# Optimization experiments

Hardware: AMD Instinct MI355X
Metric: run time of the kernel (lower is better)

Reference implementation:

```python
import jax, jax.numpy as jnp
import numpy as np

B, N, F, T, K, C, CT = 64, 307, 64, 12, 3, 64, 64
LN_EPS = 1e-5


def setup_inputs() -> dict:
    key = jax.random.key(0)
    ks = jax.random.split(key, 20)
    s = 0.1  # mild scale so sigmoid/softmax stay in a sane range
    return {
        "x": jax.random.normal(ks[0], (B, N, F, T), jnp.float32),
        "W1": jax.random.normal(ks[1], (T,), jnp.float32) * s,
        "W2": jax.random.normal(ks[2], (F, T), jnp.float32) * s,
        "W3": jax.random.normal(ks[3], (F,), jnp.float32) * s,
        "b_s": jax.random.normal(ks[4], (1, N, N), jnp.float32) * s,
        "V_s": jax.random.normal(ks[5], (N, N), jnp.float32) * s,
        "U1": jax.random.normal(ks[6], (N,), jnp.float32) * s,
        "U2": jax.random.normal(ks[7], (F, N), jnp.float32) * s,
        "U3": jax.random.normal(ks[8], (F,), jnp.float32) * s,
        "b_e": jax.random.normal(ks[9], (1, T, T), jnp.float32) * s,
        "V_e": jax.random.normal(ks[10], (T, T), jnp.float32) * s,
        "cheb": jax.random.normal(ks[11], (K, N, N), jnp.float32) * s,
        "Theta": jax.random.normal(ks[12], (K, F, C), jnp.float32) * s,
        "tconv_w": jax.random.normal(ks[13], (CT, C, 1, 3), jnp.float32) * s,
        "tconv_b": jax.random.normal(ks[14], (CT,), jnp.float32) * s,
        "rconv_w": jax.random.normal(ks[15], (CT, F, 1, 1), jnp.float32) * s,
        "rconv_b": jax.random.normal(ks[16], (CT,), jnp.float32) * s,
        "gamma": jnp.ones((CT,), jnp.float32),
        "beta": jnp.zeros((CT,), jnp.float32),
    }


def _temporal_attention(x, U1, U2, U3, b_e, V_e):
    # x: (B,N,F,T)
    lhs = jnp.einsum('bnft,n->btf', x, U1) @ U2            # (B,T,N)
    rhs = jnp.einsum('f,bnft->bnt', U3, x)                 # (B,N,T)
    prod = jnp.einsum('btn,bns->bts', lhs, rhs)            # (B,T,T)
    E = jnp.einsum('uv,bvt->but', V_e, jax.nn.sigmoid(prod + b_e))
    return jax.nn.softmax(E, axis=1)                       # (B,T,T)


def _spatial_attention(x, W1, W2, W3, b_s, V_s):
    # x: (B,N,F,T)
    lhs = jnp.einsum('bnft,t->bnf', x, W1) @ W2            # (B,N,T)
    rhs = jnp.einsum('f,bnft->btn', W3, x)                 # (B,T,N)
    prod = jnp.einsum('bnt,btm->bnm', lhs, rhs)            # (B,N,N)
    sig = jax.nn.sigmoid(prod + b_s)                       # (B,N,N)
    # torch: (V_s @ sig.T(1,2,0)).T(2,0,1) -> S[b,a,i] = sum_v V_s[i,v]*sig[b,a,v]
    S = jnp.einsum('bav,iv->bai', sig, V_s)
    return jax.nn.softmax(S, axis=1)                       # (B,N,N)


def _cheb_conv_sat(x, S, cheb, Theta):
    # x: (B,N,F,T), S: (B,N,N), cheb: (K,N,N), Theta: (K,F,C)
    A = cheb[:, None] * S[None]                            # (K,B,N,N) attention-masked polys
    # out[b,j,c,t] = sum_{k,i,f} A[k,b,i,j] * x[b,i,f,t] * Theta[k,f,c]
    rhs = jnp.einsum('kbij,bift->kbjft', A, x)             # (K,B,N,F,T)
    out = jnp.einsum('kbjft,kfc->bjct', rhs, Theta)        # (B,N,C,T)
    return jax.nn.relu(out)


def _conv2d(inp, w, b, pad):
    # inp: (B,C_in,N,T), w: (C_out,C_in,kh,kw)
    y = jax.lax.conv_general_dilated(
        inp, w, window_strides=(1, 1), padding=pad,
        dimension_numbers=('NCHW', 'OIHW', 'NCHW'))
    return y + b[None, :, None, None]


def reference(x, W1, W2, W3, b_s, V_s, U1, U2, U3, b_e, V_e,
              cheb, Theta, tconv_w, tconv_b, rconv_w, rconv_b, gamma, beta):
    b, n, f_, t = x.shape
    # temporal attention gating
    E = _temporal_attention(x, U1, U2, U3, b_e, V_e)                      # (B,T,T)
    x_TAt = (x.reshape(b, n * f_, t) @ E).reshape(b, n, f_, t)
    # spatial attention on temporally-gated signal
    S = _spatial_attention(x_TAt, W1, W2, W3, b_s, V_s)                   # (B,N,N)
    # attention-weighted Chebyshev graph conv on original x
    spatial_gcn = _cheb_conv_sat(x, S, cheb, Theta)                       # (B,N,C,T)
    # temporal conv (1,3), SAME padding along time
    tco = _conv2d(spatial_gcn.transpose(0, 2, 1, 3), tconv_w, tconv_b,
                  ((0, 0), (1, 1))).transpose(0, 2, 1, 3)                 # (B,N,CT,T)
    # 1x1 residual conv on x
    res = _conv2d(x.transpose(0, 2, 1, 3), rconv_w, rconv_b,
                  ((0, 0), (0, 0))).transpose(0, 2, 1, 3)                 # (B,N,CT,T)
    h = jax.nn.relu(res + tco)
    # LayerNorm over the filter/channel axis (axis=2)
    mu = jnp.mean(h, axis=2, keepdims=True)
    var = jnp.var(h, axis=2, keepdims=True)
    hn = (h - mu) * jax.lax.rsqrt(var + LN_EPS)
    return hn * gamma[None, None, :, None] + beta[None, None, :, None]
```

## Files before the change

kernel.cpp:

```cpp
#include <hip/hip_runtime.h>
#include <hip/hip_bf16.h>
#include <math.h>

constexpr int B = 64, N = 307, F = 64, T = 12, K = 3, C = 64, CT = 64;
constexpr float LN_EPS = 1e-5f;
constexpr int FT = F * T;

typedef float vf4 __attribute__((ext_vector_type(4)));
typedef short s16x8 __attribute__((ext_vector_type(8)));

__device__ __forceinline__ unsigned short f2bf(float f) {
    unsigned int u = __float_as_uint(f);
    unsigned int r = u + 0x7FFFu + ((u >> 16) & 1u);
    return (unsigned short)(r >> 16);
}


__global__ void k_lhs1_e(const float* __restrict__ x, const float* __restrict__ U1,
                         float* __restrict__ out) {
    int bb = blockIdx.x;
    int b = bb / 3;
    int e = (bb % 3) * 256 + threadIdx.x;
    const float* xp = x + (size_t)b * N * FT + e;
    float s = 0.f;
    for (int n = 0; n < N; n++) s += xp[(size_t)n * FT] * U1[n];
    int f = e / T, t = e % T;
    out[((size_t)b * T + t) * F + f] = s;
}

__global__ void k_xdots(const float* __restrict__ x, const float* __restrict__ U3,
                        const float* __restrict__ W3, float* __restrict__ rhs_e,
                        float* __restrict__ xw3) {
    int idx = blockIdx.x * blockDim.x + threadIdx.x;
    if (idx >= B * N * T) return;
    int t = idx % T;
    size_t bn = idx / T;
    const float* xp = x + bn * F * T + t;
    float s1 = 0.f, s2 = 0.f;
    for (int f = 0; f < F; f++) {
        float v = xp[f * T];
        s1 += U3[f] * v;
        s2 += W3[f] * v;
    }
    rhs_e[idx] = s1;
    xw3[idx] = s2;
}

__global__ void k_lhs_e(const float* __restrict__ lhs1, const float* __restrict__ U2,
                        float* __restrict__ out) {
    int idx = blockIdx.x * blockDim.x + threadIdx.x;
    if (idx >= B * T * N) return;
    int n = idx % N;
    int bt = idx / N;
    const float* lp = lhs1 + (size_t)bt * F;
    float s = 0.f;
    for (int f = 0; f < F; f++) s += lp[f] * U2[f * N + n];
    out[idx] = s;
}

__global__ void k_tatt(const float* __restrict__ lhs, const float* __restrict__ rhs,
                       const float* __restrict__ b_e, const float* __restrict__ V_e,
                       const float* __restrict__ W1, float* __restrict__ E,
                       float* __restrict__ EW1) {
    int b = blockIdx.x;
    int tid = threadIdx.x;
    __shared__ float ll[T][N + 1];
    __shared__ float rr_[T][N + 1];
    __shared__ float sig[T * T];
    __shared__ float Ev[T * T];
    __shared__ float mx[T], sm[T];
    for (int l = tid; l < T * N; l += 256) ll[l / N][l % N] = lhs[(size_t)b * T * N + l];
    for (int l = tid; l < N * T; l += 256) rr_[l % T][l / T] = rhs[(size_t)b * N * T + l];
    __syncthreads();
    if (tid < T * T) {
        int t = tid % T, u = tid / T;
        const vf4* lp4 = (const vf4*)&ll[u][0];
        const vf4* rp4 = (const vf4*)&rr_[t][0];
        float s = 0.f;
#pragma unroll 4
        for (int q = 0; q < 76; q++) {
            vf4 a = lp4[q], c = rp4[q];
            s += a[0] * c[0] + a[1] * c[1] + a[2] * c[2] + a[3] * c[3];
        }
        for (int n = 304; n < N; n++) s += ll[u][n] * rr_[t][n];
        s += b_e[u * T + t];
        sig[tid] = 1.f / (1.f + expf(-s));
    }
    __syncthreads();
    if (tid < T * T) {
        int t = tid % T, u = tid / T;
        float e = 0.f;
        for (int v = 0; v < T; v++) e += V_e[u * T + v] * sig[v * T + t];
        Ev[tid] = e;
    }
    __syncthreads();
    if (tid < T) {
        float m = -1e30f;
        for (int u = 0; u < T; u++) m = fmaxf(m, Ev[u * T + tid]);
        float s = 0.f;
        for (int u = 0; u < T; u++) s += expf(Ev[u * T + tid] - m);
        mx[tid] = m;
        sm[tid] = s;
    }
    __syncthreads();
    if (tid < T * T) {
        int t = tid % T;
        float val = expf(Ev[tid] - mx[t]) / sm[t];
        E[(size_t)b * T * T + tid] = val;
        sig[tid] = val;
    }
    __syncthreads();
    if (tid < T) {
        float s = 0.f;
        for (int t = 0; t < T; t++) s += sig[tid * T + t] * W1[t];
        EW1[(size_t)b * T + tid] = s;
    }
}


__global__ void k_lhs_sf(const float* __restrict__ x, const float* __restrict__ EW1,
                         const float* __restrict__ W2, float* __restrict__ lhs_s) {
    int bn = blockIdx.x;
    int b = bn / N;
    int tid = threadIdx.x;
    __shared__ float a[F];
    __shared__ float ew[T];
    if (tid < T) ew[tid] = EW1[(size_t)b * T + tid];
    __syncthreads();
    const float* xp = x + (size_t)bn * F * T + tid * T;
    float s = 0.f;
    for (int tp = 0; tp < T; tp++) s += xp[tp] * ew[tp];
    a[tid] = s;
    __syncthreads();
    if (tid < T) {
        float s2 = 0.f;
        for (int f = 0; f < F; f++) s2 += a[f] * W2[f * T + tid];
        lhs_s[(size_t)bn * T + tid] = s2;
    }
}

__global__ void k_rhs_s2(const float* __restrict__ xw3, const float* __restrict__ E,
                         float* __restrict__ out) {
    int idx = blockIdx.x * blockDim.x + threadIdx.x;
    if (idx >= B * T * N) return;
    int m = idx % N;
    int t = (idx / N) % T;
    int b = idx / (N * T);
    const float* xp = xw3 + ((size_t)b * N + m) * T;
    const float* Ep = E + (size_t)b * T * T + t;
    float s = 0.f;
    for (int tp = 0; tp < T; tp++) s += xp[tp] * Ep[tp * T];
    out[idx] = s;
}

constexpr int PREP_NN = N * N;
constexpr int PREP_TW = CT * C * 3;
constexpr int PREP_TH = K * F * C;
constexpr int PREP_TOT = PREP_NN + PREP_TW + PREP_TH;
constexpr int PREP_CHT = K * N * N;
constexpr int PREP_TOT2 = PREP_TOT + PREP_CHT;

__global__ void k_prep(const float* __restrict__ V, const float* __restrict__ tw,
                       const float* __restrict__ Th, const float* __restrict__ cheb,
                       float* __restrict__ VT, float* __restrict__ twT,
                       float* __restrict__ ThT, float* __restrict__ chebT) {
    int idx = blockIdx.x * blockDim.x + threadIdx.x;
    if (idx < PREP_NN) {
        int v = idx % N;
        int i = idx / N;
        VT[(size_t)v * N + i] = V[(size_t)i * N + v];
    } else if (idx < PREP_NN + PREP_TW) {
        int l = idx - PREP_NN;
        int dt = l % 3;
        int c = (l / 3) % C;
        int ct = l / (3 * C);
        twT[((size_t)dt * CT + ct) * C + c] = tw[l];
    } else if (idx < PREP_TOT) {
        int l = idx - PREP_NN - PREP_TW;
        int c = l % C;
        int f = (l / C) % F;
        int k = l / (C * F);
        ThT[((size_t)k * C + c) * F + f] = Th[l];
    } else if (idx < PREP_TOT2) {
        int l = idx - PREP_TOT;
        int i = l % N;
        int j = (l / N) % N;
        int k = l / (N * N);
        chebT[((size_t)k * N + j) * N + i] = cheb[((size_t)k * N + i) * N + j];
    }
}

constexpr int AT = 4;
constexpr int NAB = (N + AT - 1) / AT;

__global__ void k_sigS(const float* __restrict__ lhs_s, const float* __restrict__ rhs_s,
                       const float* __restrict__ b_s, const float* __restrict__ VsT,
                       float* __restrict__ S) {
    int blk = blockIdx.x;
    int b = blk / NAB;
    int a0 = (blk % NAB) * AT;
    int tid = threadIdx.x;
    __shared__ float lrow[AT][T];
    __shared__ float sig4[AT][N];
    if (tid < AT * T) {
        int a = tid / T, t = tid % T;
        lrow[a][t] = (a0 + a < N) ? lhs_s[((size_t)b * N + a0 + a) * T + t] : 0.f;
    }
    __syncthreads();
    for (int v = tid; v < N; v += 256) {
        float rv[T];
        for (int t = 0; t < T; t++) rv[t] = rhs_s[((size_t)b * T + t) * N + v];
        for (int a = 0; a < AT; a++) {
            if (a0 + a >= N) break;
            float s = 0.f;
            for (int t = 0; t < T; t++) s += lrow[a][t] * rv[t];
            s += b_s[(size_t)(a0 + a) * N + v];
            sig4[a][v] = 1.f / (1.f + expf(-s));
        }
    }
    __syncthreads();
    for (int i = tid; i < N; i += 256) {
        float s[AT] = {0.f, 0.f, 0.f, 0.f};
        for (int v = 0; v < N; v++) {
            float vt = VsT[(size_t)v * N + i];
            for (int a = 0; a < AT; a++) s[a] += sig4[a][v] * vt;
        }
        for (int a = 0; a < AT; a++)
            if (a0 + a < N) S[((size_t)b * N + a0 + a) * N + i] = s[a];
    }
}

__global__ void k_softmax_S(float* __restrict__ S) {
    int idx = blockIdx.x * blockDim.x + threadIdx.x;
    if (idx >= B * N) return;
    int b = idx / N;
    int i = idx % N;
    float* p = S + (size_t)b * N * N + i;
    float m = -1e30f;
    for (int a = 0; a < N; a++) m = fmaxf(m, p[(size_t)a * N]);
    float s = 0.f;
    for (int a = 0; a < N; a++) s += expf(p[(size_t)a * N] - m);
    float inv = 1.f / s;
    for (int a = 0; a < N; a++) p[(size_t)a * N] = expf(p[(size_t)a * N] - m) * inv;
}

__global__ void k_softT(const float* __restrict__ S, float* __restrict__ ST) {
    int b = blockIdx.x >> 1;
    int c0 = (blockIdx.x & 1) * 256;
    int tid = threadIdx.x;
    int c = c0 + tid;
    bool act = c < N;
    const float* p = S + (size_t)b * N * N + c;
    float m = -1e30f, s = 0.f;
    if (act) {
        for (int r = 0; r < N; r++) m = fmaxf(m, p[(size_t)r * N]);
        for (int r = 0; r < N; r++) s += expf(p[(size_t)r * N] - m);
    }
    float inv = act ? 1.f / s : 0.f;
    __shared__ float tile[32][257];
    float* STb = ST + (size_t)b * N * N;
    for (int r0 = 0; r0 < N; r0 += 32) {
        int rmax = min(32, N - r0);
        if (act)
            for (int rr = 0; rr < rmax; rr++)
                tile[rr][tid] = expf(p[(size_t)(r0 + rr) * N] - m) * inv;
        __syncthreads();
        for (int it = 0; it < 32; it++) {
            int cl = 8 * it + (tid >> 5);
            int cc = c0 + cl;
            int r = r0 + (tid & 31);
            if (cc < N && (tid & 31) < rmax) STb[(size_t)cc * N + r] = tile[tid & 31][cl];
        }
        __syncthreads();
    }
}


constexpr int JT = 4;
constexpr int NJB = (N + JT - 1) / JT;
constexpr int GGRID = B * NJB;
constexpr int IP = 320;

constexpr long XI_TOT = (long)B * 48 * 10 * 64;

__global__ void k_xI(const float* __restrict__ x, unsigned short* __restrict__ xI) {
    long idx = (long)blockIdx.x * 256 + threadIdx.x;
    if (idx >= XI_TOT) return;
    int lane = (int)(idx & 63);
    int ks = (int)((idx >> 6) % 10);
    int et = (int)((idx / 640) % 48);
    int b = (int)(idx / 30720);
    int col = lane & 15, kg = lane >> 4;
    int i0 = ks * 32 + kg * 8;
    int e = et * 16 + col;
    const float* xp = x + (size_t)b * N * FT + e;
    s16x8 out;
#pragma unroll
    for (int r = 0; r < 8; r++) {
        int i = i0 + r;
        out[r] = (i < N) ? (short)f2bf(xp[(size_t)i * FT]) : (short)0;
    }
    *(s16x8*)(xI + (size_t)idx * 8) = out;
}

__global__ void k_Wq16(const float* __restrict__ chebT, const float* __restrict__ ST,
                       unsigned short* __restrict__ Wq) {
    long idx = (long)blockIdx.x * 256 + threadIdx.x;
    long tot = (long)B * NJB * 12 * IP;
    if (idx >= tot) return;
    int i = (int)(idx % IP);
    int q = (int)((idx / IP) % 12);
    int jb = (int)((idx / (12L * IP)) % NJB);
    int b = (int)(idx / (12L * IP * NJB));
    int k = q >> 2, jj = q & 3, j = jb * 4 + jj;
    float w = 0.f;
    if (i < N && j < N)
        w = chebT[((size_t)k * N + j) * N + i] * ST[((size_t)b * N + j) * N + i];
    Wq[idx] = f2bf(w);
}

__global__ __launch_bounds__(256, 3) void k_gcnz_m(const unsigned short* __restrict__ xI,
                                                   const unsigned short* __restrict__ WqT,
                                                   const float* __restrict__ ThT,
                                                   float* __restrict__ sg) {
    int blk0 = blockIdx.x;
    int blk = (blk0 & 7) * (GGRID / 8) + (blk0 >> 3);
    int b = blk / NJB;
    int jb = blk % NJB;
    int j0 = jb * JT;
    int tid = threadIdx.x;
    int w = tid >> 6;
    int lane = tid & 63;
    int col = lane & 15;
    int kg = lane >> 4;

    __shared__ float zlf[3 * 3080];

    vf4 acc[12];
#pragma unroll
    for (int mt = 0; mt < 12; mt++) acc[mt] = (vf4){0.f, 0.f, 0.f, 0.f};

    const unsigned short* xb =
        xI + ((size_t)(b * 48 + w * 12) * 10) * 512 + (size_t)lane * 8;
    const unsigned short* wb =
        WqT + ((size_t)(b * NJB + jb) * 12 + (col < 12 ? col : 11)) * IP + kg * 8;

    s16x8 cx[6], nx[6], cw, nw;
    auto ldx = [&](s16x8* d, int h, int ks) {
#pragma unroll
        for (int m = 0; m < 6; m++)
            d[m] = *(const s16x8*)(xb + (size_t)((h * 6 + m) * 10 + ks) * 512);
    };

    cw = *(const s16x8*)(wb);
    ldx(cx, 0, 0);
#pragma unroll
    for (int step = 0; step < 20; step++) {
        int ks = step >> 1, h = step & 1;
        if (step < 19) {
            int ns = step + 1;
            int nks = ns >> 1, nh = ns & 1;
            nw = (nh == 0) ? *(const s16x8*)(wb + nks * 32) : cw;
            ldx(nx, nh, nks);
        }
#pragma unroll
        for (int m = 0; m < 6; m++)
            acc[h * 6 + m] =
                __builtin_amdgcn_mfma_f32_16x16x32_bf16(cw, cx[m], acc[h * 6 + m], 0, 0, 0);
        if (step < 19) {
            cw = nw;
#pragma unroll
            for (int m = 0; m < 6; m++) cx[m] = nx[m];
        }
        (void)ks;
    }

    if (kg < 3) {
#pragma unroll
        for (int mt = 0; mt < 12; mt++) {
            int e = w * 192 + mt * 16 + col;
            *(vf4*)(zlf + kg * 3080 + e * 4) = acc[mt];
        }
    }
    __syncthreads();

    if (tid < 192) {
        int t = tid % T;
        int c0 = (tid / T) * 4;
        float s[4][4];
#pragma unroll
        for (int cc = 0; cc < 4; cc++)
#pragma unroll
            for (int jj = 0; jj < 4; jj++) s[cc][jj] = 0.f;

#pragma unroll
        for (int k = 0; k < K; k++) {
            const vf4* zpk = (const vf4*)(zlf + k * 3080 + t * 4);
            const vf4* tp0 = (const vf4*)(ThT + ((size_t)k * C + c0 + 0) * F);
            const vf4* tp1 = (const vf4*)(ThT + ((size_t)k * C + c0 + 1) * F);
            const vf4* tp2 = (const vf4*)(ThT + ((size_t)k * C + c0 + 2) * F);
            const vf4* tp3 = (const vf4*)(ThT + ((size_t)k * C + c0 + 3) * F);
#pragma unroll 4
            for (int fq = 0; fq < F / 4; fq++) {
                vf4 z0 = zpk[(4 * fq + 0) * 12];
                vf4 z1 = zpk[(4 * fq + 1) * 12];
                vf4 z2 = zpk[(4 * fq + 2) * 12];
                vf4 z3 = zpk[(4 * fq + 3) * 12];
                vf4 th[4];
                th[0] = tp0[fq];
                th[1] = tp1[fq];
                th[2] = tp2[fq];
                th[3] = tp3[fq];
#pragma unroll
                for (int cc = 0; cc < 4; cc++) {
#pragma unroll
                    for (int jj = 0; jj < 4; jj++)
                        s[cc][jj] += th[cc][0] * z0[jj] + th[cc][1] * z1[jj] +
                                     th[cc][2] * z2[jj] + th[cc][3] * z3[jj];
                }
            }
        }
#pragma unroll
        for (int jj = 0; jj < 4; jj++) {
            int j = j0 + jj;
            if (j < N) {
                float* op = sg + ((size_t)b * N + j) * FT + (size_t)c0 * T + t;
                op[0 * T] = fmaxf(s[0][jj], 0.f);
                op[1 * T] = fmaxf(s[1][jj], 0.f);
                op[2 * T] = fmaxf(s[2][jj], 0.f);
                op[3 * T] = fmaxf(s[3][jj], 0.f);
            }
        }
    }
}


__global__ void k_Wp(const float* __restrict__ cheb, const float* __restrict__ S,
                     float* __restrict__ Wp) {
    long idx = (long)blockIdx.x * 256 + threadIdx.x;
    long tot = (long)B * NJB * N * 12;
    if (idx >= tot) return;
    int q = (int)(idx % 12);
    int i = (int)((idx / 12) % N);
    int jb = (int)((idx / (12L * N)) % NJB);
    int b = (int)(idx / (12L * N * NJB));
    int k = q >> 2, jj = q & 3;
    int j = jb * 4 + jj;
    float w = 0.f;
    if (j < N) w = cheb[((size_t)k * N + i) * N + j] * S[((size_t)b * N + i) * N + j];
    Wp[idx] = w;
}

__global__ __launch_bounds__(256, 4) void k_gcnz_p(const float* __restrict__ x,
                                                   const float* __restrict__ Wp,
                                                   const float* __restrict__ ThT,
                                                   float* __restrict__ sg) {
    int blk0 = blockIdx.x;
    int blk = (blk0 & 7) * (GGRID / 8) + (blk0 >> 3);
    int b = blk / NJB;
    int jb = blk % NJB;
    int j0 = jb * JT;
    int tid = threadIdx.x;

    __shared__ float zl[K][F][T][JT];

    float acc[K * JT][3];
#pragma unroll
    for (int m = 0; m < K * JT; m++)
#pragma unroll
        for (int r = 0; r < 3; r++) acc[m][r] = 0.f;

    const float* xp = x + (size_t)b * N * FT + 3 * tid;
    const float* wb = Wp + ((size_t)b * NJB + jb) * N * 12;

    float w0[12], w1[12], w2[12];
    float x0[3], x1[3], x2[3];

    auto LD = [&](float* wreg, float* xreg, int i) {
        const vf4* p = (const vf4*)(wb + (size_t)i * 12);
        vf4 a = p[0], b4 = p[1], c4 = p[2];
#pragma unroll
        for (int q = 0; q < 4; q++) {
            wreg[q] = a[q];
            wreg[4 + q] = b4[q];
            wreg[8 + q] = c4[q];
        }
        const float* xq = xp + (size_t)i * FT;
        xreg[0] = xq[0];
        xreg[1] = xq[1];
        xreg[2] = xq[2];
    };
    auto FMA = [&](const float* wreg, const float* xreg) {
#pragma unroll
        for (int m = 0; m < K * JT; m++) {
            acc[m][0] += wreg[m] * xreg[0];
            acc[m][1] += wreg[m] * xreg[1];
            acc[m][2] += wreg[m] * xreg[2];
        }
    };

    LD(w0, x0, 0);
    LD(w1, x1, 1);
    LD(w2, x2, 2);
    int i = 0;
    for (; i + 5 < N; i += 3) {
        float a0[12], a1[12], a2[12], y0[3], y1[3], y2[3];
        LD(a0, y0, i + 3);
        LD(a1, y1, i + 4);
        LD(a2, y2, i + 5);
        FMA(w0, x0);
        FMA(w1, x1);
        FMA(w2, x2);
#pragma unroll
        for (int m = 0; m < 12; m++) {
            w0[m] = a0[m];
            w1[m] = a1[m];
            w2[m] = a2[m];
        }
#pragma unroll
        for (int r = 0; r < 3; r++) {
            x0[r] = y0[r];
            x1[r] = y1[r];
            x2[r] = y2[r];
        }
    }
    FMA(w0, x0);
    FMA(w1, x1);
    FMA(w2, x2);
    for (i += 3; i < N; i++) {
        LD(w0, x0, i);
        FMA(w0, x0);
    }

#pragma unroll
    for (int r = 0; r < 3; r++) {
        int e = 3 * tid + r;
        int f = e / T, t = e % T;
#pragma unroll
        for (int m = 0; m < K * JT; m++) zl[m >> 2][f][t][m & 3] = acc[m][r];
    }
    __syncthreads();

    if (tid < 192) {
        int t = tid % T;
        int c0 = (tid / T) * 4;
        float s[4][4];
#pragma unroll
        for (int cc = 0; cc < 4; cc++)
#pragma unroll
            for (int jj = 0; jj < 4; jj++) s[cc][jj] = 0.f;

#pragma unroll
        for (int k = 0; k < K; k++) {
            const vf4* zpk = (const vf4*)&zl[k][0][t][0];
            const vf4* tp0 = (const vf4*)(ThT + ((size_t)k * C + c0 + 0) * F);
            const vf4* tp1 = (const vf4*)(ThT + ((size_t)k * C + c0 + 1) * F);
            const vf4* tp2 = (const vf4*)(ThT + ((size_t)k * C + c0 + 2) * F);
            const vf4* tp3 = (const vf4*)(ThT + ((size_t)k * C + c0 + 3) * F);
#pragma unroll 4
            for (int fq = 0; fq < F / 4; fq++) {
                vf4 z0 = zpk[(4 * fq + 0) * 12];
                vf4 z1 = zpk[(4 * fq + 1) * 12];
                vf4 z2 = zpk[(4 * fq + 2) * 12];
                vf4 z3 = zpk[(4 * fq + 3) * 12];
                vf4 th[4];
                th[0] = tp0[fq];
                th[1] = tp1[fq];
                th[2] = tp2[fq];
                th[3] = tp3[fq];
#pragma unroll
                for (int cc = 0; cc < 4; cc++) {
#pragma unroll
                    for (int jj = 0; jj < 4; jj++)
                        s[cc][jj] += th[cc][0] * z0[jj] + th[cc][1] * z1[jj] +
                                     th[cc][2] * z2[jj] + th[cc][3] * z3[jj];
                }
            }
        }
#pragma unroll
        for (int jj = 0; jj < 4; jj++) {
            int j = j0 + jj;
            if (j < N) {
                float* op = sg + ((size_t)b * N + j) * FT + (size_t)c0 * T + t;
                op[0 * T] = fmaxf(s[0][jj], 0.f);
                op[1 * T] = fmaxf(s[1][jj], 0.f);
                op[2 * T] = fmaxf(s[2][jj], 0.f);
                op[3 * T] = fmaxf(s[3][jj], 0.f);
            }
        }
    }
}


constexpr int RB = 4;
constexpr int PF = 68;

__global__ void k_rest(const float* __restrict__ x, const float* __restrict__ twT,
                       const float* __restrict__ tb, const float* __restrict__ rw,
                       const float* __restrict__ rb, const float* __restrict__ gamma,
                       const float* __restrict__ beta, float* __restrict__ io) {
    int blk = blockIdx.x;
    size_t bn0 = (size_t)blk * RB;
    int tid = threadIdx.x;

    __shared__ float xt[RB][T][PF];
    __shared__ float sgt[RB][T + 2][PF];
    __shared__ float red0[RB][T][17];
    __shared__ float red1[RB][T][17];
    __shared__ float mus[RB][T], rstds[RB][T];

    for (int l = tid; l < RB * PF; l += 192) {
        int rr = l / PF, c = l % PF;
        sgt[rr][0][c] = 0.f;
        sgt[rr][T + 1][c] = 0.f;
    }
    for (int l = tid; l < RB * FT; l += 192) {
        int rr = l / FT, rem = l % FT;
        int f = rem / T, t = rem % T;
        xt[rr][t][f] = x[(bn0 + rr) * FT + rem];
        sgt[rr][t + 1][f] = io[(bn0 + rr) * FT + rem];
    }
    __syncthreads();

    int t = tid % T;
    int cg = tid / T;
    int ct0 = cg * 4;

    float acc[RB][4];
#pragma unroll
    for (int rr = 0; rr < RB; rr++)
#pragma unroll
        for (int q = 0; q < 4; q++) acc[rr][q] = rb[ct0 + q] + tb[ct0 + q];

    {
        const vf4* w0 = (const vf4*)(rw + (size_t)(ct0 + 0) * F);
        const vf4* w1 = (const vf4*)(rw + (size_t)(ct0 + 1) * F);
        const vf4* w2 = (const vf4*)(rw + (size_t)(ct0 + 2) * F);
        const vf4* w3 = (const vf4*)(rw + (size_t)(ct0 + 3) * F);
#pragma unroll 4
        for (int fq = 0; fq < F / 4; fq++) {
            vf4 a = w0[fq], b4 = w1[fq], c4 = w2[fq], d4 = w3[fq];
#pragma unroll
            for (int rr = 0; rr < RB; rr++) {
                vf4 v = *(const vf4*)(&xt[rr][t][fq * 4]);
                acc[rr][0] += a[0] * v[0] + a[1] * v[1] + a[2] * v[2] + a[3] * v[3];
                acc[rr][1] += b4[0] * v[0] + b4[1] * v[1] + b4[2] * v[2] + b4[3] * v[3];
                acc[rr][2] += c4[0] * v[0] + c4[1] * v[1] + c4[2] * v[2] + c4[3] * v[3];
                acc[rr][3] += d4[0] * v[0] + d4[1] * v[1] + d4[2] * v[2] + d4[3] * v[3];
            }
        }
    }
#pragma unroll
    for (int dt = 0; dt < 3; dt++) {
        const vf4* w0 = (const vf4*)(twT + ((size_t)dt * CT + ct0 + 0) * C);
        const vf4* w1 = (const vf4*)(twT + ((size_t)dt * CT + ct0 + 1) * C);
        const vf4* w2 = (const vf4*)(twT + ((size_t)dt * CT + ct0 + 2) * C);
        const vf4* w3 = (const vf4*)(twT + ((size_t)dt * CT + ct0 + 3) * C);
#pragma unroll 4
        for (int fq = 0; fq < C / 4; fq++) {
            vf4 a = w0[fq], b4 = w1[fq], c4 = w2[fq], d4 = w3[fq];
#pragma unroll
            for (int rr = 0; rr < RB; rr++) {
                vf4 v = *(const vf4*)(&sgt[rr][t + dt][fq * 4]);
                acc[rr][0] += a[0] * v[0] + a[1] * v[1] + a[2] * v[2] + a[3] * v[3];
                acc[rr][1] += b4[0] * v[0] + b4[1] * v[1] + b4[2] * v[2] + b4[3] * v[3];
                acc[rr][2] += c4[0] * v[0] + c4[1] * v[1] + c4[2] * v[2] + c4[3] * v[3];
                acc[rr][3] += d4[0] * v[0] + d4[1] * v[1] + d4[2] * v[2] + d4[3] * v[3];
            }
        }
    }

#pragma unroll
    for (int rr = 0; rr < RB; rr++) {
        float ps = 0.f;
#pragma unroll
        for (int q = 0; q < 4; q++) {
            float h = fmaxf(acc[rr][q], 0.f);
            acc[rr][q] = h;
            ps += h;
        }
        red0[rr][t][cg] = ps;
    }
    __syncthreads();
    if (tid < RB * T) {
        int rr = tid / T, tt = tid % T;
        float m = 0.f;
#pragma unroll 4
        for (int g = 0; g < 16; g++) m += red0[rr][tt][g];
        mus[rr][tt] = m * (1.f / CT);
    }
    __syncthreads();
#pragma unroll
    for (int rr = 0; rr < RB; rr++) {
        float m = mus[rr][t];
        float pv = 0.f;
#pragma unroll
        for (int q = 0; q < 4; q++) {
            float d = acc[rr][q] - m;
            pv += d * d;
        }
        red1[rr][t][cg] = pv;
    }
    __syncthreads();
    if (tid < RB * T) {
        int rr = tid / T, tt = tid % T;
        float v = 0.f;
#pragma unroll 4
        for (int g = 0; g < 16; g++) v += red1[rr][tt][g];
        rstds[rr][tt] = rsqrtf(v * (1.f / CT) + LN_EPS);
    }
    __syncthreads();
#pragma unroll
    for (int rr = 0; rr < RB; rr++) {
        float m = mus[rr][t], rs = rstds[rr][t];
        float* iop = io + (bn0 + rr) * FT;
#pragma unroll
        for (int q = 0; q < 4; q++) {
            int ct = ct0 + q;
            iop[ct * T + t] = (acc[rr][q] - m) * rs * gamma[ct] + beta[ct];
        }
    }
}


extern "C" void kernel_launch(void* const* d_in, const int* in_sizes, int n_in,
                              void* d_out, int out_size, void* d_ws, size_t ws_size,
                              hipStream_t stream) {
    const float* x     = (const float*)d_in[0];
    const float* W1    = (const float*)d_in[1];
    const float* W2    = (const float*)d_in[2];
    const float* W3    = (const float*)d_in[3];
    const float* b_s   = (const float*)d_in[4];
    const float* V_s   = (const float*)d_in[5];
    const float* U1    = (const float*)d_in[6];
    const float* U2    = (const float*)d_in[7];
    const float* U3    = (const float*)d_in[8];
    const float* b_e   = (const float*)d_in[9];
    const float* V_e   = (const float*)d_in[10];
    const float* cheb  = (const float*)d_in[11];
    const float* Theta = (const float*)d_in[12];
    const float* tw    = (const float*)d_in[13];
    const float* tb    = (const float*)d_in[14];
    const float* rw    = (const float*)d_in[15];
    const float* rb    = (const float*)d_in[16];
    const float* gam   = (const float*)d_in[17];
    const float* bet   = (const float*)d_in[18];
    float* out = (float*)d_out;

    float* ws = (float*)d_ws;
    size_t off = 0;
    auto alloc = [&](size_t n) { float* p = ws + off; off += n; return p; };
    float* VsT = alloc((size_t)N * N);
    float* twT = alloc((size_t)CT * C * 3);
    float* ThT = alloc((size_t)K * F * C);
    size_t base_end = off;
    float* lhs1_e = alloc((size_t)B * T * F);
    float* lhs_e  = alloc((size_t)B * T * N);
    float* rhs_e  = alloc((size_t)B * N * T);
    float* Ebuf   = alloc((size_t)B * T * T);
    float* EW1    = alloc((size_t)B * T);
    float* xw3    = alloc((size_t)B * N * T);
    float* lhs_s  = alloc((size_t)B * N * T);
    float* rhs_s  = alloc((size_t)B * T * N);
    float* Sb     = alloc((size_t)B * N * N);
    size_t poolA_end = off;

    size_t wq_fl = (size_t)B * NJB * 12 * IP / 2;
    unsigned short* WqT = (unsigned short*)(ws + base_end);
    size_t off2 = base_end + wq_fl;
    if (off2 < poolA_end) off2 = poolA_end;
    float* chebT = ws + off2; off2 += (size_t)K * N * N;
    float* SbT = ws + off2; off2 += (size_t)B * N * N;
    unsigned short* xI = (unsigned short*)(ws + off2);
    off2 += (size_t)XI_TOT * 8 / 2;
    bool useM = ws_size >= off2 * sizeof(float);

    size_t wp_off = (poolA_end + 3) & ~(size_t)3;
    float* Wp = ws + wp_off;
    bool useWp = !useM && ws_size >= (wp_off + (size_t)B * NJB * N * 12) * sizeof(float);

    auto g = [](long n) { return dim3((unsigned)((n + 255) / 256)); };

    k_prep<<<g(useM ? (long)PREP_TOT2 : (long)PREP_TOT), 256, 0, stream>>>(
        V_s, tw, Theta, cheb, VsT, twT, ThT, chebT);
    if (useM) k_xI<<<g(XI_TOT), 256, 0, stream>>>(x, xI);

    k_lhs1_e<<<dim3(B * 3), 256, 0, stream>>>(x, U1, lhs1_e);
    k_xdots<<<g((long)B * N * T), 256, 0, stream>>>(x, U3, W3, rhs_e, xw3);
    k_lhs_e<<<g((long)B * T * N), 256, 0, stream>>>(lhs1_e, U2, lhs_e);
    k_tatt<<<B, 256, 0, stream>>>(lhs_e, rhs_e, b_e, V_e, W1, Ebuf, EW1);

    k_lhs_sf<<<B * N, 64, 0, stream>>>(x, EW1, W2, lhs_s);
    k_rhs_s2<<<g((long)B * T * N), 256, 0, stream>>>(xw3, Ebuf, rhs_s);
    k_sigS<<<B * NAB, 256, 0, stream>>>(lhs_s, rhs_s, b_s, VsT, Sb);

    if (useM) {
        k_softT<<<dim3(B * 2), 256, 0, stream>>>(Sb, SbT);
        k_Wq16<<<g((long)B * NJB * 12 * IP), 256, 0, stream>>>(chebT, SbT, WqT);
        k_gcnz_m<<<GGRID, 256, 0, stream>>>(xI, WqT, ThT, out);
    } else if (useWp) {
        k_softmax_S<<<g((long)B * N), 256, 0, stream>>>(Sb);
        k_Wp<<<g((long)B * NJB * N * 12), 256, 0, stream>>>(cheb, Sb, Wp);
        k_gcnz_p<<<GGRID, 256, 0, stream>>>(x, Wp, ThT, out);
    }

    k_rest<<<(B * N) / RB, 192, 0, stream>>>(x, twT, tb, rw, rb, gam, bet, out);
}
```

Baseline: 921.3 us.

## Split GCN MFMA work across 8 waves and pack 4 nodes per lhs_sf block

```diff
diff --git a/kernel.cpp b/kernel.cpp
--- a/kernel.cpp
+++ b/kernel.cpp
@@ -120,22 +120,26 @@
 
 __global__ void k_lhs_sf(const float* __restrict__ x, const float* __restrict__ EW1,
                          const float* __restrict__ W2, float* __restrict__ lhs_s) {
-    int bn = blockIdx.x;
-    int b = bn / N;
-    int tid = threadIdx.x;
-    __shared__ float a[F];
-    __shared__ float ew[T];
-    if (tid < T) ew[tid] = EW1[(size_t)b * T + tid];
-    __syncthreads();
-    const float* xp = x + (size_t)bn * F * T + tid * T;
+    int blk = blockIdx.x;
+    int sub = threadIdx.x >> 6;
+    int ft = threadIdx.x & 63;
+    size_t bn = (size_t)blk * 4 + sub;
+    int b = (int)(bn / N);
+    __shared__ float a[4][F];
+    __shared__ float ew[4][T];
+    if (ft < T) ew[sub][ft] = EW1[(size_t)b * T + ft];
+    __syncthreads();
+    const float* xp = x + bn * FT + ft * T;
     float s = 0.f;
-    for (int tp = 0; tp < T; tp++) s += xp[tp] * ew[tp];
-    a[tid] = s;
-    __syncthreads();
-    if (tid < T) {
+#pragma unroll
+    for (int tp = 0; tp < T; tp++) s += xp[tp] * ew[sub][tp];
+    a[sub][ft] = s;
+    __syncthreads();
+    if (ft < T) {
         float s2 = 0.f;
-        for (int f = 0; f < F; f++) s2 += a[f] * W2[f * T + tid];
-        lhs_s[(size_t)bn * T + tid] = s2;
+#pragma unroll 8
+        for (int f = 0; f < F; f++) s2 += a[sub][f] * W2[f * T + ft];
+        lhs_s[bn * T + ft] = s2;
     }
 }
 
@@ -319,7 +323,7 @@
     Wq[idx] = f2bf(w);
 }
 
-__global__ __launch_bounds__(256, 3) void k_gcnz_m(const unsigned short* __restrict__ xI,
+__global__ __launch_bounds__(512, 6) void k_gcnz_m(const unsigned short* __restrict__ xI,
                                                    const unsigned short* __restrict__ WqT,
                                                    const float* __restrict__ ThT,
                                                    float* __restrict__ sg) {
@@ -336,50 +340,30 @@
 
     __shared__ float zlf[3 * 3080];
 
-    vf4 acc[12];
-#pragma unroll
-    for (int mt = 0; mt < 12; mt++) acc[mt] = (vf4){0.f, 0.f, 0.f, 0.f};
+    vf4 acc[6];
+#pragma unroll
+    for (int m = 0; m < 6; m++) acc[m] = (vf4){0.f, 0.f, 0.f, 0.f};
 
     const unsigned short* xb =
-        xI + ((size_t)(b * 48 + w * 12) * 10) * 512 + (size_t)lane * 8;
+        xI + ((size_t)(b * 48 + w * 6) * 10) * 512 + (size_t)lane * 8;
     const unsigned short* wb =
         WqT + ((size_t)(b * NJB + jb) * 12 + (col < 12 ? col : 11)) * IP + kg * 8;
 
-    s16x8 cx[6], nx[6], cw, nw;
-    auto ldx = [&](s16x8* d, int h, int ks) {
-#pragma unroll
-        for (int m = 0; m < 6; m++)
-            d[m] = *(const s16x8*)(xb + (size_t)((h * 6 + m) * 10 + ks) * 512);
-    };
-
-    cw = *(const s16x8*)(wb);
-    ldx(cx, 0, 0);
-#pragma unroll
-    for (int step = 0; step < 20; step++) {
-        int ks = step >> 1, h = step & 1;
-        if (step < 19) {
-            int ns = step + 1;
-            int nks = ns >> 1, nh = ns & 1;
-            nw = (nh == 0) ? *(const s16x8*)(wb + nks * 32) : cw;
-            ldx(nx, nh, nks);
-        }
-#pragma unroll
-        for (int m = 0; m < 6; m++)
-            acc[h * 6 + m] =
-                __builtin_amdgcn_mfma_f32_16x16x32_bf16(cw, cx[m], acc[h * 6 + m], 0, 0, 0);
-        if (step < 19) {
-            cw = nw;
-#pragma unroll
-            for (int m = 0; m < 6; m++) cx[m] = nx[m];
-        }
-        (void)ks;
+#pragma unroll 2
+    for (int ks = 0; ks < 10; ks++) {
+        s16x8 wf = *(const s16x8*)(wb + ks * 32);
+#pragma unroll
+        for (int m = 0; m < 6; m++) {
+            s16x8 xf = *(const s16x8*)(xb + (size_t)(m * 10 + ks) * 512);
+            acc[m] = __builtin_amdgcn_mfma_f32_16x16x32_bf16(wf, xf, acc[m], 0, 0, 0);
+        }
     }
 
     if (kg < 3) {
 #pragma unroll
-        for (int mt = 0; mt < 12; mt++) {
-            int e = w * 192 + mt * 16 + col;
-            *(vf4*)(zlf + kg * 3080 + e * 4) = acc[mt];
+        for (int m = 0; m < 6; m++) {
+            int e = (w * 6 + m) * 16 + col;
+            *(vf4*)(zlf + kg * 3080 + e * 4) = acc[m];
         }
     }
     __syncthreads();
@@ -790,14 +774,14 @@
     k_lhs_e<<<g((long)B * T * N), 256, 0, stream>>>(lhs1_e, U2, lhs_e);
     k_tatt<<<B, 256, 0, stream>>>(lhs_e, rhs_e, b_e, V_e, W1, Ebuf, EW1);
 
-    k_lhs_sf<<<B * N, 64, 0, stream>>>(x, EW1, W2, lhs_s);
+    k_lhs_sf<<<dim3((B * N) / 4), 256, 0, stream>>>(x, EW1, W2, lhs_s);
     k_rhs_s2<<<g((long)B * T * N), 256, 0, stream>>>(xw3, Ebuf, rhs_s);
     k_sigS<<<B * NAB, 256, 0, stream>>>(lhs_s, rhs_s, b_s, VsT, Sb);
 
     if (useM) {
         k_softT<<<dim3(B * 2), 256, 0, stream>>>(Sb, SbT);
         k_Wq16<<<g((long)B * NJB * 12 * IP), 256, 0, stream>>>(chebT, SbT, WqT);
-        k_gcnz_m<<<GGRID, 256, 0, stream>>>(xI, WqT, ThT, out);
+        k_gcnz_m<<<GGRID, 512, 0, stream>>>(xI, WqT, ThT, out);
     } else if (useWp) {
         k_softmax_S<<<g((long)B * N), 256, 0, stream>>>(Sb);
         k_Wp<<<g((long)B * NJB * N * 12), 256, 0, stream>>>(cheb, Sb, Wp);
```

After: 1.198 ms. +30.1%, slower.
